# Kernel tuning notes

Measured on AMD Instinct MI355X. Metric: run time of the kernel, lower is better.

## Reference

```python
import jax, jax.numpy as jnp
import numpy as np

N, E, D, C, L = 50000, 800000, 128, 10, 3
TAU = 0.5
EPS = 1e-5


def _ln(h, g, b):
    m = jnp.mean(h, axis=-1, keepdims=True)
    v = jnp.mean((h - m) ** 2, axis=-1, keepdims=True)
    return (h - m) * jax.lax.rsqrt(v + EPS) * g + b


def _gumbel_hard(logits, gnoise, tau):
    # gumbel_softmax(hard=True): straight-through one-hot of softmax((logits+g)/tau)
    y_soft = jax.nn.softmax((logits + gnoise) / tau, axis=-1)
    idx = jnp.argmax(y_soft, axis=-1)
    y_hard = jax.nn.one_hot(idx, logits.shape[-1], dtype=y_soft.dtype)
    return jax.lax.stop_gradient(y_hard - y_soft) + y_soft


def setup_inputs() -> dict:
    key = jax.random.key(0)
    ks = jax.random.split(key, 20)
    s = lambda *sh: 1.0 / np.sqrt(sh[0])
    inp = {
        "x": jax.random.normal(ks[0], (N, D), jnp.float32),
        "edge_index": jax.random.randint(ks[1], (2, E), 0, N, jnp.int64),
        # encoder (node_encoder Linear in_dim->env_dim)
        "W_enc": jax.random.normal(ks[2], (D, D), jnp.float32) * s(D),
        "b_enc": jnp.zeros((D,), jnp.float32),
        # shared hidden LayerNorm
        "ln_g": jnp.ones((D,), jnp.float32),
        "ln_b": jnp.zeros((D,), jnp.float32),
        # env GNN layers (root / neighbor weights + bias), L layers
        "Wr": jax.random.normal(ks[3], (L, D, D), jnp.float32) * s(D),
        "Wn": jax.random.normal(ks[4], (L, D, D), jnp.float32) * s(D),
        "bl": jnp.zeros((L, D), jnp.float32),
        # in/out action nets (1 layer each, env_dim -> 2 logits)
        "Wa_in_r": jax.random.normal(ks[5], (D, 2), jnp.float32) * s(D),
        "Wa_in_n": jax.random.normal(ks[6], (D, 2), jnp.float32) * s(D),
        "ba_in": jnp.zeros((2,), jnp.float32),
        "Wa_out_r": jax.random.normal(ks[7], (D, 2), jnp.float32) * s(D),
        "Wa_out_n": jax.random.normal(ks[8], (D, 2), jnp.float32) * s(D),
        "ba_out": jnp.zeros((2,), jnp.float32),
        # decoder (dec_num_layers=1 -> single Linear env_dim -> num_classes)
        "W_dec": jax.random.normal(ks[9], (D, C), jnp.float32) * s(D),
        "b_dec": jnp.zeros((C,), jnp.float32),
        # pre-sampled Gumbel noise per layer for in/out action gates
        "gin": jax.random.gumbel(ks[10], (L, N, 2), jnp.float32),
        "gout": jax.random.gumbel(ks[11], (L, N, 2), jnp.float32),
    }
    return inp


def reference(x, edge_index, W_enc, b_enc, ln_g, ln_b, Wr, Wn, bl,
              Wa_in_r, Wa_in_n, ba_in, Wa_out_r, Wa_out_n, ba_out,
              W_dec, b_dec, gin, gout):
    u, v = edge_index[0], edge_index[1]
    n = x.shape[0]
    # node encoder + (use_encoders=False) dropout(0)+act
    h = jax.nn.relu(x @ W_enc + b_enc)
    node_states = []
    for l in range(L):
        hn = _ln(h, ln_g, ln_b)
        # unweighted neighbor aggregation shared by both action nets
        agg = jax.ops.segment_sum(hn[u], v, num_segments=n)  # [N, D]
        in_logits = hn @ Wa_in_r + agg @ Wa_in_n + ba_in
        out_logits = hn @ Wa_out_r + agg @ Wa_out_n + ba_out
        in_p = _gumbel_hard(in_logits, gin[l], TAU)
        out_p = _gumbel_hard(out_logits, gout[l], TAU)
        # edge gate: listen prob of target * broadcast prob of source
        ew = in_p[v, 0] * out_p[u, 0]  # [E]
        aggw = jax.ops.segment_sum(ew[:, None] * hn[u], v, num_segments=n)
        out = jax.nn.relu(hn @ Wr[l] + aggw @ Wn[l] + bl[l])
        # node state bookkeeping: 0 standard, 1 broadcast-only, 2 listen-only, 3 isolated
        act = jax.lax.stop_gradient(ew)
        is_b = (jax.ops.segment_max(act, u, num_segments=n) > 0.5).astype(jnp.int32)
        is_l = (jax.ops.segment_max(act, v, num_segments=n) > 0.5).astype(jnp.int32)
        node_states.append(3 - 2 * is_b - is_l)
        h = hn + out  # skip connection (onto the normalized x, as in the source)
    h = _ln(h, ln_g, ln_b)
    result = h @ W_dec + b_dec
    return result, jnp.stack(node_states)
```

## Files before the change

kernel.cpp:

```cpp
#include <hip/hip_runtime.h>

#define DIM 128
#define NCLS 10

__global__ void k_hist(const int* __restrict__ ei, int E, int* __restrict__ deg) {
    int e = blockIdx.x * 256 + threadIdx.x;
    if (e < E) atomicAdd(&deg[ei[E + e]], 1);
}

__global__ void k_scan1(const int* __restrict__ deg, int* __restrict__ row_start,
                        int* __restrict__ bsum, int n) {
    int tid = threadIdx.x;
    int base = blockIdx.x * 1024 + tid * 4;
    int v0 = 0, v1 = 0, v2 = 0, v3 = 0;
    if (base + 3 < n) {
        int4 t = *(const int4*)(deg + base);
        v0 = t.x; v1 = t.y; v2 = t.z; v3 = t.w;
    } else {
        if (base + 0 < n) v0 = deg[base + 0];
        if (base + 1 < n) v1 = deg[base + 1];
        if (base + 2 < n) v2 = deg[base + 2];
        if (base + 3 < n) v3 = deg[base + 3];
    }
    int s = v0 + v1 + v2 + v3;
    int lane = tid & 63, w = tid >> 6;
    int inc = s;
#pragma unroll
    for (int o = 1; o < 64; o <<= 1) {
        int t = __shfl_up(inc, o);
        if (lane >= o) inc += t;
    }
    __shared__ int wsum[4];
    if (lane == 63) wsum[w] = inc;
    __syncthreads();
    int woff = 0;
    for (int i = 0; i < w; i++) woff += wsum[i];
    int run = woff + inc - s;
    if (base + 0 < n) row_start[base + 0] = run; run += v0;
    if (base + 1 < n) row_start[base + 1] = run; run += v1;
    if (base + 2 < n) row_start[base + 2] = run; run += v2;
    if (base + 3 < n) row_start[base + 3] = run;
    if (tid == 0) bsum[blockIdx.x] = wsum[0] + wsum[1] + wsum[2] + wsum[3];
}

__global__ void k_scan2(int* __restrict__ bsum, int nb) {
    int tid = threadIdx.x;
    if (nb <= 64) {
        int v = (tid < nb) ? bsum[tid] : 0;
        int inc = v;
#pragma unroll
        for (int o = 1; o < 64; o <<= 1) {
            int t = __shfl_up(inc, o);
            if (tid >= o) inc += t;
        }
        if (tid < nb) bsum[tid] = inc - v;
    } else if (tid == 0) {
        int acc = 0;
        for (int i = 0; i < nb; i++) { int t = bsum[i]; bsum[i] = acc; acc += t; }
    }
}

__global__ void k_scan3(int* __restrict__ row_start, int* __restrict__ cursor,
                        const int* __restrict__ bsum, int n, int E) {
    int i = blockIdx.x * 256 + threadIdx.x;
    if (i < n) {
        int r = row_start[i] + bsum[i >> 10];
        row_start[i] = r;
        cursor[i] = r;
    }
    if (i == n) row_start[n] = E;
}

__global__ void k_fill(const int* __restrict__ ei, int E, int* __restrict__ cursor,
                       int* __restrict__ csr) {
    int e = blockIdx.x * 256 + threadIdx.x;
    if (e < E) {
        int u = ei[e], v = ei[E + e];
        int pos = atomicAdd(&cursor[v], 1);
        csr[pos] = u;
    }
}

__global__ void k_action(const float* __restrict__ proj, const int* __restrict__ row_start,
                         const int* __restrict__ csr,
                         const float* __restrict__ bain, const float* __restrict__ baon,
                         const float* __restrict__ gin_l, const float* __restrict__ gout_l,
                         int* __restrict__ in_bit, int* __restrict__ out_bit,
                         int* __restrict__ is_b, int* __restrict__ is_l, int n) {
    int v = blockIdx.x * 256 + threadIdx.x;
    if (v >= n) return;
    is_b[v] = 0; is_l[v] = 0;
    int b0 = row_start[v], b1 = row_start[v + 1];
    double a0 = 0.0, a1 = 0.0, a2 = 0.0, a3 = 0.0;
    for (int e = b0; e < b1; e++) {
        int u = csr[e];
        float4 p = *(const float4*)(proj + (size_t)u * 8);
        a0 += p.x; a1 += p.y; a2 += p.z; a3 += p.w;
    }
    float4 r = *(const float4*)(proj + (size_t)v * 8 + 4);
    float2 gi = *(const float2*)(gin_l + (size_t)v * 2);
    float2 go = *(const float2*)(gout_l + (size_t)v * 2);
    float li0 = (float)a0 + r.x + bain[0] + gi.x;
    float li1 = (float)a1 + r.y + bain[1] + gi.y;
    float lo0 = (float)a2 + r.z + baon[0] + go.x;
    float lo1 = (float)a3 + r.w + baon[1] + go.y;
    in_bit[v]  = (li0 >= li1) ? 1 : 0;
    out_bit[v] = (lo0 >= lo1) ? 1 : 0;
}

__global__ void k_state_edges(const int* __restrict__ ei, int E,
                              const int* __restrict__ in_bit, const int* __restrict__ out_bit,
                              int* __restrict__ is_b, int* __restrict__ is_l) {
    int e = blockIdx.x * 256 + threadIdx.x;
    if (e < E) {
        int u = ei[e], v = ei[E + e];
        if (in_bit[v] & out_bit[u]) { is_b[u] = 1; is_l[v] = 1; }
    }
}

__global__ void k_aggw(const float* __restrict__ hn, const int* __restrict__ row_start,
                       const int* __restrict__ csr, const int* __restrict__ in_bit,
                       const int* __restrict__ out_bit,
                       const int* __restrict__ is_b, const int* __restrict__ is_l,
                       float* __restrict__ aggw, float* __restrict__ out_states_l, int n) {
    int wid = (blockIdx.x * 256 + threadIdx.x) >> 6;
    int lane = threadIdx.x & 63;
    if (wid >= n) return;
    if (lane == 0)
        out_states_l[wid] = (float)(3 - 2 * is_b[wid] - is_l[wid]);
    int d0 = lane * 2;
    float ax = 0.f, ay = 0.f;
    if (in_bit[wid]) {
        int base = row_start[wid], end = row_start[wid + 1];
        for (int off = base; off < end; off += 64) {
            int m = min(64, end - off);
            int myu = 0, myb = 0;
            if (lane < m) { myu = csr[off + lane]; myb = out_bit[myu]; }
            unsigned long long mask = __ballot(myb != 0);
            while (mask) {
                int i = __ffsll((unsigned long long)mask) - 1;
                mask &= mask - 1;
                int u = __shfl(myu, i);
                float2 t = *(const float2*)(hn + (size_t)u * DIM + d0);
                ax += t.x; ay += t.y;
            }
        }
    }
    ((float2*)(aggw + (size_t)wid * DIM))[lane] = make_float2(ax, ay);
}

template <int HAS_B, int SKIP, int DO_LN, int DO_PROJ>
__global__ void k_gemm(const float* __restrict__ A, const float* __restrict__ W1,
                       const float* __restrict__ B, const float* __restrict__ W2,
                       const float* __restrict__ bias,
                       const float* __restrict__ ln_g, const float* __restrict__ ln_b,
                       const float* __restrict__ Wain, const float* __restrict__ Waon,
                       const float* __restrict__ Wair, const float* __restrict__ Waor,
                       float* __restrict__ out, float* __restrict__ proj, int n) {
    __shared__ float sW[32][128];
    __shared__ float sA[32][36];
    int tid = threadIdx.x;
    int rowBase = blockIdx.x * 32;
    int ty = tid >> 4, tx = tid & 15;
    int c0 = tx * 4, c1 = 64 + tx * 4;
    float acc[2][8];
#pragma unroll
    for (int i = 0; i < 2; i++)
#pragma unroll
        for (int j = 0; j < 8; j++) acc[i][j] = 0.f;

    for (int p = 0; p < 1 + HAS_B; p++) {
        const float* Ap = p ? B : A;
        const float* Wp = p ? W2 : W1;
        for (int kc = 0; kc < DIM; kc += 32) {
            __syncthreads();
            {
                const float4* src = (const float4*)(Wp + kc * DIM);
                float4* dst = (float4*)(&sW[0][0]);
#pragma unroll
                for (int i = 0; i < 4; i++) dst[tid + i * 256] = src[tid + i * 256];
            }
            {
                int r = tid >> 3, c4 = (tid & 7) * 4;
                float4 va = (rowBase + r < n)
                    ? *(const float4*)(Ap + (size_t)(rowBase + r) * DIM + kc + c4)
                    : make_float4(0.f, 0.f, 0.f, 0.f);
                *(float4*)&sA[r][c4] = va;
            }
            __syncthreads();
#pragma unroll
            for (int kk = 0; kk < 32; kk += 4) {
                float4 a0 = *(const float4*)&sA[ty][kk];
                float4 a1 = *(const float4*)&sA[ty + 16][kk];
                float a0v[4] = {a0.x, a0.y, a0.z, a0.w};
                float a1v[4] = {a1.x, a1.y, a1.z, a1.w};
#pragma unroll
                for (int q = 0; q < 4; q++) {
                    float4 w0 = *(const float4*)&sW[kk + q][c0];
                    float4 w1 = *(const float4*)&sW[kk + q][c1];
                    float wv[8] = {w0.x, w0.y, w0.z, w0.w, w1.x, w1.y, w1.z, w1.w};
#pragma unroll
                    for (int j = 0; j < 8; j++) {
                        acc[0][j] += a0v[q] * wv[j];
                        acc[1][j] += a1v[q] * wv[j];
                    }
                }
            }
        }
    }

    float4 bias0 = *(const float4*)&bias[c0];
    float4 bias1 = *(const float4*)&bias[c1];
    float bv[8] = {bias0.x, bias0.y, bias0.z, bias0.w, bias1.x, bias1.y, bias1.z, bias1.w};
    float gv[8], bbv[8];
    if (DO_LN) {
        float4 g0 = *(const float4*)&ln_g[c0];
        float4 g1 = *(const float4*)&ln_g[c1];
        float4 lb0 = *(const float4*)&ln_b[c0];
        float4 lb1 = *(const float4*)&ln_b[c1];
        gv[0]=g0.x; gv[1]=g0.y; gv[2]=g0.z; gv[3]=g0.w; gv[4]=g1.x; gv[5]=g1.y; gv[6]=g1.z; gv[7]=g1.w;
        bbv[0]=lb0.x; bbv[1]=lb0.y; bbv[2]=lb0.z; bbv[3]=lb0.w; bbv[4]=lb1.x; bbv[5]=lb1.y; bbv[6]=lb1.z; bbv[7]=lb1.w;
    }

#pragma unroll
    for (int i = 0; i < 2; i++) {
        int r = rowBase + ty + i * 16;
        if (r >= n) continue;
        float v[8];
        if (SKIP) {
            float4 s0 = *(const float4*)(A + (size_t)r * DIM + c0);
            float4 s1 = *(const float4*)(A + (size_t)r * DIM + c1);
            float sv[8] = {s0.x, s0.y, s0.z, s0.w, s1.x, s1.y, s1.z, s1.w};
#pragma unroll
            for (int j = 0; j < 8; j++) v[j] = fmaxf(acc[i][j] + bv[j], 0.f) + sv[j];
        } else {
#pragma unroll
            for (int j = 0; j < 8; j++) v[j] = fmaxf(acc[i][j] + bv[j], 0.f);
        }
        if (DO_LN) {
            float s = 0.f, q = 0.f;
#pragma unroll
            for (int j = 0; j < 8; j++) { s += v[j]; q += v[j] * v[j]; }
#pragma unroll
            for (int o = 1; o < 16; o <<= 1) { s += __shfl_xor(s, o); q += __shfl_xor(q, o); }
            float m = s * (1.f / DIM);
            float var = q * (1.f / DIM) - m * m;
            float inv = rsqrtf(var + 1e-5f);
#pragma unroll
            for (int j = 0; j < 8; j++) v[j] = (v[j] - m) * inv * gv[j] + bbv[j];
        }
        *(float4*)(out + (size_t)r * DIM + c0) = make_float4(v[0], v[1], v[2], v[3]);
        *(float4*)(out + (size_t)r * DIM + c1) = make_float4(v[4], v[5], v[6], v[7]);

        if (DO_PROJ) {
            float pv[8];
            auto dotw = [&](const float* Wm, float& p0, float& p1) {
                float4 q0 = *(const float4*)(Wm + c0 * 2);
                float4 q1 = *(const float4*)(Wm + c0 * 2 + 4);
                float4 q2 = *(const float4*)(Wm + c1 * 2);
                float4 q3 = *(const float4*)(Wm + c1 * 2 + 4);
                p0 = v[0]*q0.x + v[1]*q0.z + v[2]*q1.x + v[3]*q1.z
                   + v[4]*q2.x + v[5]*q2.z + v[6]*q3.x + v[7]*q3.z;
                p1 = v[0]*q0.y + v[1]*q0.w + v[2]*q1.y + v[3]*q1.w
                   + v[4]*q2.y + v[5]*q2.w + v[6]*q3.y + v[7]*q3.w;
            };
            dotw(Wain, pv[0], pv[1]);
            dotw(Waon, pv[2], pv[3]);
            dotw(Wair, pv[4], pv[5]);
            dotw(Waor, pv[6], pv[7]);
#pragma unroll
            for (int o = 1; o < 16; o <<= 1)
#pragma unroll
                for (int j = 0; j < 8; j++) pv[j] += __shfl_xor(pv[j], o);
            if (tx == 0) {
                *(float4*)(proj + (size_t)r * 8)     = make_float4(pv[0], pv[1], pv[2], pv[3]);
                *(float4*)(proj + (size_t)r * 8 + 4) = make_float4(pv[4], pv[5], pv[6], pv[7]);
            }
        }
    }
}

__global__ void k_final(const float* __restrict__ hn, const float* __restrict__ Wdec,
                        const float* __restrict__ bdec, float* __restrict__ out, int n) {
    __shared__ float sWd[NCLS * DIM];
    int tid = threadIdx.x;
    for (int i = tid; i < NCLS * DIM; i += 256) {
        int d = i / NCLS, c = i % NCLS;
        sWd[c * DIM + d] = Wdec[i];
    }
    __syncthreads();
    int wid = (blockIdx.x * 256 + threadIdx.x) >> 6;
    int lane = threadIdx.x & 63;
    if (wid >= n) return;
    int d0 = lane * 2;
    float2 v = ((const float2*)(hn + (size_t)wid * DIM))[lane];
    float p[NCLS];
#pragma unroll
    for (int c = 0; c < NCLS; c++) {
        float2 w = *(const float2*)(&sWd[c * DIM + d0]);
        p[c] = v.x * w.x + v.y * w.y;
    }
#pragma unroll
    for (int o = 32; o; o >>= 1)
#pragma unroll
        for (int c = 0; c < NCLS; c++) p[c] += __shfl_xor(p[c], o);
    if (lane == 0) {
#pragma unroll
        for (int c = 0; c < NCLS; c++) out[(size_t)wid * NCLS + c] = p[c] + bdec[c];
    }
}

extern "C" void kernel_launch(void* const* d_in, const int* in_sizes, int n_in,
                              void* d_out, int out_size, void* d_ws, size_t ws_size,
                              hipStream_t stream) {
    const float* x      = (const float*)d_in[0];
    const int*   ei     = (const int*)d_in[1];
    const float* W_enc  = (const float*)d_in[2];
    const float* b_enc  = (const float*)d_in[3];
    const float* ln_g   = (const float*)d_in[4];
    const float* ln_b   = (const float*)d_in[5];
    const float* Wr     = (const float*)d_in[6];
    const float* Wn     = (const float*)d_in[7];
    const float* bl     = (const float*)d_in[8];
    const float* Wair   = (const float*)d_in[9];
    const float* Wain   = (const float*)d_in[10];
    const float* bain   = (const float*)d_in[11];
    const float* Waor   = (const float*)d_in[12];
    const float* Waon   = (const float*)d_in[13];
    const float* baon   = (const float*)d_in[14];
    const float* W_dec  = (const float*)d_in[15];
    const float* b_dec  = (const float*)d_in[16];
    const float* gin    = (const float*)d_in[17];
    const float* gout   = (const float*)d_in[18];

    int n = in_sizes[0] / DIM;
    int E = in_sizes[1] / 2;
    const int L = 3;

    char* wsp = (char*)d_ws;
    auto alloc = [&](size_t bytes) { char* p = wsp; wsp += (bytes + 255) / 256 * 256; return p; };
    float* hn   = (float*)alloc((size_t)n * DIM * 4);
    float* aggw = (float*)alloc((size_t)n * DIM * 4);
    float* proj = (float*)alloc((size_t)n * 8 * 4);
    int* deg       = (int*)alloc((size_t)n * 4);
    int* row_start = (int*)alloc((size_t)(n + 1) * 4);
    int* cursor    = (int*)alloc((size_t)n * 4);
    int* csr       = (int*)alloc((size_t)E * 4);
    int* in_bit    = (int*)alloc((size_t)n * 4);
    int* out_bit   = (int*)alloc((size_t)n * 4);
    int* bsum      = (int*)alloc((size_t)256 * 4);
    int* is_bl     = (int*)alloc((size_t)2 * n * 4);
    int* is_b = is_bl;
    int* is_l = is_bl + n;

    float* out_res    = (float*)d_out;
    float* out_states = out_res + (size_t)n * NCLS;

    int ebl = (E + 255) / 256;
    int nbl = (n + 255) / 256;
    int wbl = (n + 3) / 4;
    int gbl = (n + 31) / 32;
    int nb  = (n + 1023) / 1024;

    hipMemsetAsync(deg, 0, (size_t)n * 4, stream);
    k_hist<<<ebl, 256, 0, stream>>>(ei, E, deg);
    k_scan1<<<nb, 256, 0, stream>>>(deg, row_start, bsum, n);
    k_scan2<<<1, 64, 0, stream>>>(bsum, nb);
    k_scan3<<<(n + 256) / 256, 256, 0, stream>>>(row_start, cursor, bsum, n, E);
    k_fill<<<ebl, 256, 0, stream>>>(ei, E, cursor, csr);

    k_gemm<0, 0, 1, 1><<<gbl, 256, 0, stream>>>(x, W_enc, nullptr, nullptr, b_enc,
                                                ln_g, ln_b, Wain, Waon, Wair, Waor,
                                                hn, proj, n);

    for (int l = 0; l < L; l++) {
        k_action<<<nbl, 256, 0, stream>>>(proj, row_start, csr, bain, baon,
                                          gin + (size_t)l * n * 2, gout + (size_t)l * n * 2,
                                          in_bit, out_bit, is_b, is_l, n);
        k_state_edges<<<ebl, 256, 0, stream>>>(ei, E, in_bit, out_bit, is_b, is_l);
        k_aggw<<<wbl, 256, 0, stream>>>(hn, row_start, csr, in_bit, out_bit,
                                        is_b, is_l, aggw, out_states + (size_t)l * n, n);
        if (l + 1 < L)
            k_gemm<1, 1, 1, 1><<<gbl, 256, 0, stream>>>(hn, Wr + (size_t)l * DIM * DIM,
                                                        aggw, Wn + (size_t)l * DIM * DIM,
                                                        bl + (size_t)l * DIM,
                                                        ln_g, ln_b, Wain, Waon, Wair, Waor,
                                                        hn, proj, n);
        else
            k_gemm<1, 1, 1, 0><<<gbl, 256, 0, stream>>>(hn, Wr + (size_t)l * DIM * DIM,
                                                        aggw, Wn + (size_t)l * DIM * DIM,
                                                        bl + (size_t)l * DIM,
                                                        ln_g, ln_b, Wain, Waon, Wair, Waor,
                                                        hn, proj, n);
    }
    k_final<<<wbl, 256, 0, stream>>>(hn, W_dec, b_dec, out_res, n);
}
```

Baseline: 532.3 us.

## Fuse state bookkeeping into aggregation, decoder into final GEMM, enlarge GEMM tile

Removes the per-layer edge pass that set broadcast/listen flags. The flags are now derived inside the gated aggregation kernel, and node states are written from the following GEMM epilogue. The decoder projection moves into the last GEMM's epilogue, which also skips writing h, and the GEMM tile grows from 32 to 128 rows per block so each weight chunk is reused by more rows. Aggregation accumulates in double. This adds register pressure from the 8x8 accumulator, and the flag scatters (is_b writes) race benignly across waves.

```diff
diff --git a/kernel.cpp b/kernel.cpp
--- a/kernel.cpp
+++ b/kernel.cpp
@@ -86,10 +86,10 @@
                          const float* __restrict__ bain, const float* __restrict__ baon,
                          const float* __restrict__ gin_l, const float* __restrict__ gout_l,
                          int* __restrict__ in_bit, int* __restrict__ out_bit,
-                         int* __restrict__ is_b, int* __restrict__ is_l, int n) {
+                         int* __restrict__ is_b, int n) {
     int v = blockIdx.x * 256 + threadIdx.x;
     if (v >= n) return;
-    is_b[v] = 0; is_l[v] = 0;
+    is_b[v] = 0;
     int b0 = row_start[v], b1 = row_start[v + 1];
     double a0 = 0.0, a1 = 0.0, a2 = 0.0, a3 = 0.0;
     for (int e = b0; e < b1; e++) {
@@ -108,28 +108,17 @@
     out_bit[v] = (lo0 >= lo1) ? 1 : 0;
 }
 
-__global__ void k_state_edges(const int* __restrict__ ei, int E,
-                              const int* __restrict__ in_bit, const int* __restrict__ out_bit,
-                              int* __restrict__ is_b, int* __restrict__ is_l) {
-    int e = blockIdx.x * 256 + threadIdx.x;
-    if (e < E) {
-        int u = ei[e], v = ei[E + e];
-        if (in_bit[v] & out_bit[u]) { is_b[u] = 1; is_l[v] = 1; }
-    }
-}
-
 __global__ void k_aggw(const float* __restrict__ hn, const int* __restrict__ row_start,
                        const int* __restrict__ csr, const int* __restrict__ in_bit,
                        const int* __restrict__ out_bit,
-                       const int* __restrict__ is_b, const int* __restrict__ is_l,
-                       float* __restrict__ aggw, float* __restrict__ out_states_l, int n) {
+                       int* __restrict__ is_b, int* __restrict__ is_l,
+                       float* __restrict__ aggw, int n) {
     int wid = (blockIdx.x * 256 + threadIdx.x) >> 6;
     int lane = threadIdx.x & 63;
     if (wid >= n) return;
-    if (lane == 0)
-        out_states_l[wid] = (float)(3 - 2 * is_b[wid] - is_l[wid]);
     int d0 = lane * 2;
-    float ax = 0.f, ay = 0.f;
+    double ax = 0.0, ay = 0.0;
+    int anyg = 0;
     if (in_bit[wid]) {
         int base = row_start[wid], end = row_start[wid + 1];
         for (int off = base; off < end; off += 64) {
@@ -137,35 +126,42 @@
             int myu = 0, myb = 0;
             if (lane < m) { myu = csr[off + lane]; myb = out_bit[myu]; }
             unsigned long long mask = __ballot(myb != 0);
+            anyg |= (mask != 0ull);
             while (mask) {
                 int i = __ffsll((unsigned long long)mask) - 1;
                 mask &= mask - 1;
                 int u = __shfl(myu, i);
+                if (lane == 0) is_b[u] = 1;
                 float2 t = *(const float2*)(hn + (size_t)u * DIM + d0);
                 ax += t.x; ay += t.y;
             }
         }
     }
-    ((float2*)(aggw + (size_t)wid * DIM))[lane] = make_float2(ax, ay);
-}
-
-template <int HAS_B, int SKIP, int DO_LN, int DO_PROJ>
+    if (lane == 0) is_l[wid] = anyg;
+    ((float2*)(aggw + (size_t)wid * DIM))[lane] = make_float2((float)ax, (float)ay);
+}
+
+template <int HAS_B, int SKIP, int DO_LN, int DO_PROJ, int DO_STATES, int DO_DEC, int WRITE_H>
+__launch_bounds__(256, 4)
 __global__ void k_gemm(const float* __restrict__ A, const float* __restrict__ W1,
                        const float* __restrict__ B, const float* __restrict__ W2,
                        const float* __restrict__ bias,
                        const float* __restrict__ ln_g, const float* __restrict__ ln_b,
                        const float* __restrict__ Wain, const float* __restrict__ Waon,
                        const float* __restrict__ Wair, const float* __restrict__ Waor,
-                       float* __restrict__ out, float* __restrict__ proj, int n) {
+                       const int* __restrict__ is_b, const int* __restrict__ is_l,
+                       const float* __restrict__ Wdec, const float* __restrict__ bdec,
+                       float* __restrict__ out, float* __restrict__ proj,
+                       float* __restrict__ states_l, float* __restrict__ dec_out, int n) {
     __shared__ float sW[32][128];
-    __shared__ float sA[32][36];
+    __shared__ float sA[128][36];
     int tid = threadIdx.x;
-    int rowBase = blockIdx.x * 32;
+    int rowBase = blockIdx.x * 128;
     int ty = tid >> 4, tx = tid & 15;
     int c0 = tx * 4, c1 = 64 + tx * 4;
-    float acc[2][8];
-#pragma unroll
-    for (int i = 0; i < 2; i++)
+    float acc[8][8];
+#pragma unroll
+    for (int i = 0; i < 8; i++)
 #pragma unroll
         for (int j = 0; j < 8; j++) acc[i][j] = 0.f;
 
@@ -178,35 +174,46 @@
                 const float4* src = (const float4*)(Wp + kc * DIM);
                 float4* dst = (float4*)(&sW[0][0]);
 #pragma unroll
-                for (int i = 0; i < 4; i++) dst[tid + i * 256] = src[tid + i * 256];
-            }
-            {
-                int r = tid >> 3, c4 = (tid & 7) * 4;
-                float4 va = (rowBase + r < n)
-                    ? *(const float4*)(Ap + (size_t)(rowBase + r) * DIM + kc + c4)
-                    : make_float4(0.f, 0.f, 0.f, 0.f);
-                *(float4*)&sA[r][c4] = va;
+                for (int i = 0; i < 4; i++) {
+                    int j = i * 256 + tid;
+                    dst[j] = src[j];
+                    int r = j >> 3, c4 = (j & 7) * 4;
+                    float4 va = (rowBase + r < n)
+                        ? *(const float4*)(Ap + (size_t)(rowBase + r) * DIM + kc + c4)
+                        : make_float4(0.f, 0.f, 0.f, 0.f);
+                    *(float4*)&sA[r][c4] = va;
+                }
             }
             __syncthreads();
 #pragma unroll
             for (int kk = 0; kk < 32; kk += 4) {
-                float4 a0 = *(const float4*)&sA[ty][kk];
-                float4 a1 = *(const float4*)&sA[ty + 16][kk];
-                float a0v[4] = {a0.x, a0.y, a0.z, a0.w};
-                float a1v[4] = {a1.x, a1.y, a1.z, a1.w};
+                float4 a[8];
+#pragma unroll
+                for (int i = 0; i < 8; i++) a[i] = *(const float4*)&sA[i * 16 + ty][kk];
 #pragma unroll
                 for (int q = 0; q < 4; q++) {
                     float4 w0 = *(const float4*)&sW[kk + q][c0];
                     float4 w1 = *(const float4*)&sW[kk + q][c1];
                     float wv[8] = {w0.x, w0.y, w0.z, w0.w, w1.x, w1.y, w1.z, w1.w};
 #pragma unroll
-                    for (int j = 0; j < 8; j++) {
-                        acc[0][j] += a0v[q] * wv[j];
-                        acc[1][j] += a1v[q] * wv[j];
+                    for (int i = 0; i < 8; i++) {
+                        float av[4] = {a[i].x, a[i].y, a[i].z, a[i].w};
+#pragma unroll
+                        for (int j = 0; j < 8; j++) acc[i][j] += av[q] * wv[j];
                     }
                 }
             }
         }
+    }
+
+    float* sWd = (float*)&sW[0][0];
+    if (DO_DEC) {
+        __syncthreads();
+        for (int i = tid; i < NCLS * DIM; i += 256) {
+            int d = i / NCLS, c = i % NCLS;
+            sWd[c * DIM + d] = Wdec[i];
+        }
+        __syncthreads();
     }
 
     float4 bias0 = *(const float4*)&bias[c0];
@@ -223,8 +230,8 @@
     }
 
 #pragma unroll
-    for (int i = 0; i < 2; i++) {
-        int r = rowBase + ty + i * 16;
+    for (int i = 0; i < 8; i++) {
+        int r = rowBase + i * 16 + ty;
         if (r >= n) continue;
         float v[8];
         if (SKIP) {
@@ -249,9 +256,13 @@
 #pragma unroll
             for (int j = 0; j < 8; j++) v[j] = (v[j] - m) * inv * gv[j] + bbv[j];
         }
-        *(float4*)(out + (size_t)r * DIM + c0) = make_float4(v[0], v[1], v[2], v[3]);
-        *(float4*)(out + (size_t)r * DIM + c1) = make_float4(v[4], v[5], v[6], v[7]);
-
+        if (WRITE_H) {
+            *(float4*)(out + (size_t)r * DIM + c0) = make_float4(v[0], v[1], v[2], v[3]);
+            *(float4*)(out + (size_t)r * DIM + c1) = make_float4(v[4], v[5], v[6], v[7]);
+        }
+        if (DO_STATES) {
+            if (tx == 0) states_l[r] = (float)(3 - 2 * is_b[r] - is_l[r]);
+        }
         if (DO_PROJ) {
             float pv[8];
             auto dotw = [&](const float* Wm, float& p0, float& p1) {
@@ -277,36 +288,24 @@
                 *(float4*)(proj + (size_t)r * 8 + 4) = make_float4(pv[4], pv[5], pv[6], pv[7]);
             }
         }
-    }
-}
-
-__global__ void k_final(const float* __restrict__ hn, const float* __restrict__ Wdec,
-                        const float* __restrict__ bdec, float* __restrict__ out, int n) {
-    __shared__ float sWd[NCLS * DIM];
-    int tid = threadIdx.x;
-    for (int i = tid; i < NCLS * DIM; i += 256) {
-        int d = i / NCLS, c = i % NCLS;
-        sWd[c * DIM + d] = Wdec[i];
-    }
-    __syncthreads();
-    int wid = (blockIdx.x * 256 + threadIdx.x) >> 6;
-    int lane = threadIdx.x & 63;
-    if (wid >= n) return;
-    int d0 = lane * 2;
-    float2 v = ((const float2*)(hn + (size_t)wid * DIM))[lane];
-    float p[NCLS];
-#pragma unroll
-    for (int c = 0; c < NCLS; c++) {
-        float2 w = *(const float2*)(&sWd[c * DIM + d0]);
-        p[c] = v.x * w.x + v.y * w.y;
-    }
-#pragma unroll
-    for (int o = 32; o; o >>= 1)
-#pragma unroll
-        for (int c = 0; c < NCLS; c++) p[c] += __shfl_xor(p[c], o);
-    if (lane == 0) {
-#pragma unroll
-        for (int c = 0; c < NCLS; c++) out[(size_t)wid * NCLS + c] = p[c] + bdec[c];
+        if (DO_DEC) {
+            float p[NCLS];
+#pragma unroll
+            for (int c = 0; c < NCLS; c++) {
+                float4 wd0 = *(const float4*)&sWd[c * DIM + c0];
+                float4 wd1 = *(const float4*)&sWd[c * DIM + c1];
+                p[c] = v[0]*wd0.x + v[1]*wd0.y + v[2]*wd0.z + v[3]*wd0.w
+                     + v[4]*wd1.x + v[5]*wd1.y + v[6]*wd1.z + v[7]*wd1.w;
+            }
+#pragma unroll
+            for (int o = 1; o < 16; o <<= 1)
+#pragma unroll
+                for (int c = 0; c < NCLS; c++) p[c] += __shfl_xor(p[c], o);
+            if (tx == 0) {
+#pragma unroll
+                for (int c = 0; c < NCLS; c++) dec_out[(size_t)r * NCLS + c] = p[c] + bdec[c];
+            }
+        }
     }
 }
 
@@ -349,9 +348,8 @@
     int* in_bit    = (int*)alloc((size_t)n * 4);
     int* out_bit   = (int*)alloc((size_t)n * 4);
     int* bsum      = (int*)alloc((size_t)256 * 4);
-    int* is_bl     = (int*)alloc((size_t)2 * n * 4);
-    int* is_b = is_bl;
-    int* is_l = is_bl + n;
+    int* is_b      = (int*)alloc((size_t)n * 4);
+    int* is_l      = (int*)alloc((size_t)n * 4);
 
     float* out_res    = (float*)d_out;
     float* out_states = out_res + (size_t)n * NCLS;
@@ -359,7 +357,7 @@
     int ebl = (E + 255) / 256;
     int nbl = (n + 255) / 256;
     int wbl = (n + 3) / 4;
-    int gbl = (n + 31) / 32;
+    int gbl = (n + 127) / 128;
     int nb  = (n + 1023) / 1024;
 
     hipMemsetAsync(deg, 0, (size_t)n * 4, stream);
@@ -369,29 +367,29 @@
     k_scan3<<<(n + 256) / 256, 256, 0, stream>>>(row_start, cursor, bsum, n, E);
     k_fill<<<ebl, 256, 0, stream>>>(ei, E, cursor, csr);
 
-    k_gemm<0, 0, 1, 1><<<gbl, 256, 0, stream>>>(x, W_enc, nullptr, nullptr, b_enc,
-                                                ln_g, ln_b, Wain, Waon, Wair, Waor,
-                                                hn, proj, n);
+    k_gemm<0, 0, 1, 1, 0, 0, 1><<<gbl, 256, 0, stream>>>(
+        x, W_enc, nullptr, nullptr, b_enc, ln_g, ln_b,
+        Wain, Waon, Wair, Waor, nullptr, nullptr, nullptr, nullptr,
+        hn, proj, nullptr, nullptr, n);
 
     for (int l = 0; l < L; l++) {
         k_action<<<nbl, 256, 0, stream>>>(proj, row_start, csr, bain, baon,
                                           gin + (size_t)l * n * 2, gout + (size_t)l * n * 2,
-                                          in_bit, out_bit, is_b, is_l, n);
-        k_state_edges<<<ebl, 256, 0, stream>>>(ei, E, in_bit, out_bit, is_b, is_l);
+                                          in_bit, out_bit, is_b, n);
         k_aggw<<<wbl, 256, 0, stream>>>(hn, row_start, csr, in_bit, out_bit,
-                                        is_b, is_l, aggw, out_states + (size_t)l * n, n);
-        if (l + 1 < L)
-            k_gemm<1, 1, 1, 1><<<gbl, 256, 0, stream>>>(hn, Wr + (size_t)l * DIM * DIM,
-                                                        aggw, Wn + (size_t)l * DIM * DIM,
-                                                        bl + (size_t)l * DIM,
-                                                        ln_g, ln_b, Wain, Waon, Wair, Waor,
-                                                        hn, proj, n);
-        else
-            k_gemm<1, 1, 1, 0><<<gbl, 256, 0, stream>>>(hn, Wr + (size_t)l * DIM * DIM,
-                                                        aggw, Wn + (size_t)l * DIM * DIM,
-                                                        bl + (size_t)l * DIM,
-                                                        ln_g, ln_b, Wain, Waon, Wair, Waor,
-                                                        hn, proj, n);
-    }
-    k_final<<<wbl, 256, 0, stream>>>(hn, W_dec, b_dec, out_res, n);
-}
+                                        is_b, is_l, aggw, n);
+        if (l + 1 < L) {
+            k_gemm<1, 1, 1, 1, 1, 0, 1><<<gbl, 256, 0, stream>>>(
+                hn, Wr + (size_t)l * DIM * DIM, aggw, Wn + (size_t)l * DIM * DIM,
+                bl + (size_t)l * DIM, ln_g, ln_b,
+                Wain, Waon, Wair, Waor, is_b, is_l, nullptr, nullptr,
+                hn, proj, out_states + (size_t)l * n, nullptr, n);
+        } else {
+            k_gemm<1, 1, 1, 0, 1, 1, 0><<<gbl, 256, 0, stream>>>(
+                hn, Wr + (size_t)l * DIM * DIM, aggw, Wn + (size_t)l * DIM * DIM,
+                bl + (size_t)l * DIM, ln_g, ln_b,
+                Wain, Waon, Wair, Waor, is_b, is_l, W_dec, b_dec,
+                hn, nullptr, out_states + (size_t)l * n, out_res, n);
+        }
+    }
+}
```

Result: slower. 1.032 ms (+93.9%).
